# Kernel tuning notes

Measured on AMD Instinct MI355X. Metric: run time of the kernel, lower is better.

Reference implementation:

```python
import jax, jax.numpy as jnp
import numpy as np
import math

B, H, S, D = 2, 16, 2048, 64
DROP_P = 0.1


def setup_inputs() -> dict:
    key = jax.random.key(0)
    k1, k2 = jax.random.split(key)
    x1 = jax.random.normal(k1, (B, H, S, D), dtype=jnp.float32)  # queries
    x2 = jax.random.normal(k2, (B, H, S, D), dtype=jnp.float32)  # keys == values
    return {"x1": x1, "x2": x2}


def reference(x1, x2):
    # qk = x1 @ x2^T, scaled by 1/sqrt(head_dim)
    inv_scale = math.sqrt(x1.shape[-1])
    scores = jnp.einsum('bhqd,bhkd->bhqk', x1, x2) / inv_scale  # [B,H,S,S]
    probs = jax.nn.softmax(scores, axis=-1)
    # F.dropout(p=0.1) in training mode: deterministic jax mask with fixed key
    keep = jax.random.bernoulli(jax.random.key(42), 1.0 - DROP_P, probs.shape)
    probs = jnp.where(keep, probs / (1.0 - DROP_P), 0.0)
    out = jnp.einsum('bhqk,bhkd->bhqd', probs, x2)  # [B,H,S,D]
    return out
```

## Files before the change

### kernel.cpp

```cpp
#include <hip/hip_runtime.h>
#include <hip/hip_bf16.h>
#include <math.h>

#define BATCH 2
#define NHEAD 16
#define SLEN  2048
#define DH    64
#define WAVES 4
#define QW    16
#define QB    (WAVES*QW)
#define KB    64
#define PSTRIDE 68
#define MFIX  16.0f

typedef __attribute__((ext_vector_type(8))) short bf16x8;
typedef __attribute__((ext_vector_type(4))) float f32x4;

__device__ __forceinline__ unsigned rotl32(unsigned x, unsigned d) {
    return __builtin_amdgcn_alignbit(x, x, 32u - d);
}

__device__ __forceinline__ unsigned threefry_bits(unsigned i) {
    const unsigned k0 = 0u, k1 = 42u;
    const unsigned ks[3] = { k0, k1, k0 ^ k1 ^ 0x1BD11BDAu };
    unsigned x0 = 0u + ks[0];
    unsigned x1 = i  + ks[1];
#pragma unroll
    for (int g = 0; g < 5; ++g) {
        if ((g & 1) == 0) {
            x0 += x1; x1 = rotl32(x1, 13u); x1 ^= x0;
            x0 += x1; x1 = rotl32(x1, 15u); x1 ^= x0;
            x0 += x1; x1 = rotl32(x1, 26u); x1 ^= x0;
            x0 += x1; x1 = rotl32(x1,  6u); x1 ^= x0;
        } else {
            x0 += x1; x1 = rotl32(x1, 17u); x1 ^= x0;
            x0 += x1; x1 = rotl32(x1, 29u); x1 ^= x0;
            x0 += x1; x1 = rotl32(x1, 16u); x1 ^= x0;
            x0 += x1; x1 = rotl32(x1, 24u); x1 ^= x0;
        }
        x0 += ks[(g + 1) % 3];
        x1 += ks[(g + 2) % 3] + (unsigned)(g + 1);
    }
    return x0 ^ x1;
}

__device__ __forceinline__ int keep(unsigned flat) {
    return threefry_bits(flat) < 3865470464u;
}

__device__ __forceinline__ short f2bf(float f) {
    __hip_bfloat16 h = __float2bfloat16(f);
    return *reinterpret_cast<short*>(&h);
}

__global__ __launch_bounds__(256)
void attn_mfma_kernel(const float* __restrict__ Q,
                      const float* __restrict__ KV,
                      float* __restrict__ O) {
    __shared__ bf16x8 s_k[KB * 8];
    __shared__ bf16x8 s_vt[DH * 9];
    __shared__ float s_p[WAVES][QW][PSTRIDE];

    const int tid  = threadIdx.x;
    const int wave = tid >> 6;
    const int lane = tid & 63;
    const int g    = lane >> 4;
    const int lc   = lane & 15;

    const int blk = blockIdx.x;
    const int bh  = blk >> 5;
    const int q0  = (blk & 31) * QB + wave * QW;

    const float* Qb = Q  + ((size_t)bh * SLEN + q0) * DH;
    const float* Kb = KV + (size_t)bh * SLEN * DH;

    const float qscale = 0.125f * 1.4426950408889634f;
    bf16x8 qa[2];
#pragma unroll
    for (int h = 0; h < 2; ++h) {
        const float* qp = Qb + (size_t)lc * DH + 32 * h + g * 8;
        float4 f0 = *(const float4*)qp;
        float4 f1 = *(const float4*)(qp + 4);
        qa[h][0] = f2bf(f0.x * qscale); qa[h][1] = f2bf(f0.y * qscale);
        qa[h][2] = f2bf(f0.z * qscale); qa[h][3] = f2bf(f0.w * qscale);
        qa[h][4] = f2bf(f1.x * qscale); qa[h][5] = f2bf(f1.y * qscale);
        qa[h][6] = f2bf(f1.z * qscale); qa[h][7] = f2bf(f1.w * qscale);
    }

    f32x4 oacc[4];
#pragma unroll
    for (int t = 0; t < 4; ++t) oacc[t] = (f32x4){0.f, 0.f, 0.f, 0.f};
    float l[4] = { 0.f, 0.f, 0.f, 0.f };

    const unsigned rowbase = ((unsigned)bh * SLEN + (unsigned)(q0 + g * 4)) * SLEN;
    const unsigned fib = rowbase + (unsigned)lc;

    const int kr0 = tid >> 3;
    const int kc0 = tid & 7;
    const int vd  = tid & 63;
    const int vw  = tid >> 6;

    for (int k0 = 0; k0 < SLEN; k0 += KB) {
        __syncthreads();

#pragma unroll
        for (int rr = 0; rr < 2; ++rr) {
            const int row = kr0 + rr * 32;
            const float* src = Kb + (size_t)(k0 + row) * DH + kc0 * 8;
            float4 f0 = *(const float4*)src;
            float4 f1 = *(const float4*)(src + 4);
            bf16x8 v;
            v[0] = f2bf(f0.x); v[1] = f2bf(f0.y);
            v[2] = f2bf(f0.z); v[3] = f2bf(f0.w);
            v[4] = f2bf(f1.x); v[5] = f2bf(f1.y);
            v[6] = f2bf(f1.z); v[7] = f2bf(f1.w);
            s_k[row * 8 + (kc0 ^ (row & 7))] = v;
        }
#pragma unroll
        for (int rr = 0; rr < 2; ++rr) {
            const int w = vw + rr * 4;
            bf16x8 v;
#pragma unroll
            for (int j = 0; j < 8; ++j)
                v[j] = f2bf(Kb[(size_t)(k0 + w * 8 + j) * DH + vd]);
            s_vt[vd * 9 + w] = v;
        }
        __syncthreads();

        f32x4 sarr[4];
#pragma unroll
        for (int tt = 0; tt < 4; ++tt) {
            bf16x8 kb0 = s_k[(tt * 16 + lc) * 8 + (g       ^ (lc & 7))];
            bf16x8 kb1 = s_k[(tt * 16 + lc) * 8 + ((4 + g) ^ (lc & 7))];
            f32x4 acc = (f32x4){-MFIX, -MFIX, -MFIX, -MFIX};
            acc = __builtin_amdgcn_mfma_f32_16x16x32_bf16(qa[0], kb0, acc, 0, 0, 0);
            sarr[tt] = __builtin_amdgcn_mfma_f32_16x16x32_bf16(qa[1], kb1, acc, 0, 0, 0);
        }

#pragma unroll
        for (int i = 0; i < 4; ++i) {
            float p0 = __builtin_amdgcn_exp2f(sarr[0][i]);
            float p1 = __builtin_amdgcn_exp2f(sarr[1][i]);
            float p2 = __builtin_amdgcn_exp2f(sarr[2][i]);
            float p3 = __builtin_amdgcn_exp2f(sarr[3][i]);
            l[i] += (p0 + p1) + (p2 + p3);

            const unsigned fi = fib + (unsigned)i * SLEN + (unsigned)k0;
            if (!keep(fi))       p0 = 0.f;
            if (!keep(fi + 16u)) p1 = 0.f;
            if (!keep(fi + 32u)) p2 = 0.f;
            if (!keep(fi + 48u)) p3 = 0.f;
            float* pr = &s_p[wave][g * 4 + i][0];
            pr[lc]      = p0;
            pr[lc + 16] = p1;
            pr[lc + 32] = p2;
            pr[lc + 48] = p3;
        }

        const float* pp = &s_p[wave][lc][0];
        float4 pf0 = *(const float4*)(pp + g * 8);
        float4 pf1 = *(const float4*)(pp + g * 8 + 4);
        float4 pf2 = *(const float4*)(pp + 32 + g * 8);
        float4 pf3 = *(const float4*)(pp + 32 + g * 8 + 4);
        bf16x8 pa0, pa1;
        pa0[0] = f2bf(pf0.x); pa0[1] = f2bf(pf0.y);
        pa0[2] = f2bf(pf0.z); pa0[3] = f2bf(pf0.w);
        pa0[4] = f2bf(pf1.x); pa0[5] = f2bf(pf1.y);
        pa0[6] = f2bf(pf1.z); pa0[7] = f2bf(pf1.w);
        pa1[0] = f2bf(pf2.x); pa1[1] = f2bf(pf2.y);
        pa1[2] = f2bf(pf2.z); pa1[3] = f2bf(pf2.w);
        pa1[4] = f2bf(pf3.x); pa1[5] = f2bf(pf3.y);
        pa1[6] = f2bf(pf3.z); pa1[7] = f2bf(pf3.w);

#pragma unroll
        for (int t = 0; t < 4; ++t) {
            bf16x8 vb0 = s_vt[(t * 16 + lc) * 9 + g];
            bf16x8 vb1 = s_vt[(t * 16 + lc) * 9 + 4 + g];
            oacc[t] = __builtin_amdgcn_mfma_f32_16x16x32_bf16(pa0, vb0, oacc[t], 0, 0, 0);
            oacc[t] = __builtin_amdgcn_mfma_f32_16x16x32_bf16(pa1, vb1, oacc[t], 0, 0, 0);
        }
    }

#pragma unroll
    for (int i = 0; i < 4; ++i) {
        l[i] += __shfl_xor(l[i], 1);
        l[i] += __shfl_xor(l[i], 2);
        l[i] += __shfl_xor(l[i], 4);
        l[i] += __shfl_xor(l[i], 8);
    }

#pragma unroll
    for (int i = 0; i < 4; ++i) {
        float sc = 1.0f / (l[i] * 0.9f);
        float* orow = O + ((size_t)bh * SLEN + (size_t)(q0 + g * 4 + i)) * DH;
        orow[lc]      = oacc[0][i] * sc;
        orow[16 + lc] = oacc[1][i] * sc;
        orow[32 + lc] = oacc[2][i] * sc;
        orow[48 + lc] = oacc[3][i] * sc;
    }
}

extern "C" void kernel_launch(void* const* d_in, const int* in_sizes, int n_in,
                              void* d_out, int out_size, void* d_ws, size_t ws_size,
                              hipStream_t stream) {
    const float* x1 = (const float*)d_in[0];
    const float* x2 = (const float*)d_in[1];
    float* out = (float*)d_out;
    const int nblocks = BATCH * NHEAD * (SLEN / QB);
    attn_mfma_kernel<<<dim3(nblocks), dim3(256), 0, stream>>>(x1, x2, out);
}
```

Before: 298.0 us.

## Prefetch next K/V tile into registers and stage P as bf16 in LDS

Global loads of the next 64-key K/V tile are issued into registers right after the current tile is written to shared memory, so their latency overlaps the QK^T, softmax/dropout and PV work. The probability tile is converted to bf16 before the shared-memory store and read back as bf16x8 vectors, halving LDS traffic and removing per-element conversions after the readback. The prefetch adds register pressure, which may lower occupancy, and the last iteration does a wasted reload of tile 0.

```diff
diff --git a/kernel.cpp b/kernel.cpp
--- a/kernel.cpp
+++ b/kernel.cpp
@@ -10,7 +10,7 @@
 #define QW    16
 #define QB    (WAVES*QW)
 #define KB    64
-#define PSTRIDE 68
+#define PSTR  72
 #define MFIX  16.0f
 
 typedef __attribute__((ext_vector_type(8))) short bf16x8;
@@ -59,7 +59,7 @@
                       float* __restrict__ O) {
     __shared__ bf16x8 s_k[KB * 8];
     __shared__ bf16x8 s_vt[DH * 9];
-    __shared__ float s_p[WAVES][QW][PSTRIDE];
+    __shared__ __align__(16) short s_p[WAVES][QW][PSTR];
 
     const int tid  = threadIdx.x;
     const int wave = tid >> 6;
@@ -100,20 +100,38 @@
     const int vd  = tid & 63;
     const int vw  = tid >> 6;
 
+    float4 kpre[2][2];
+    float  vpre[2][8];
+
+    auto LOADT = [&](int kt) {
+#pragma unroll
+        for (int rr = 0; rr < 2; ++rr) {
+            const float* src = Kb + (size_t)(kt + kr0 + rr * 32) * DH + kc0 * 8;
+            kpre[rr][0] = *(const float4*)src;
+            kpre[rr][1] = *(const float4*)(src + 4);
+        }
+#pragma unroll
+        for (int rr = 0; rr < 2; ++rr) {
+            const int w = vw + rr * 4;
+#pragma unroll
+            for (int j = 0; j < 8; ++j)
+                vpre[rr][j] = Kb[(size_t)(kt + w * 8 + j) * DH + vd];
+        }
+    };
+
+    LOADT(0);
+
     for (int k0 = 0; k0 < SLEN; k0 += KB) {
         __syncthreads();
 
 #pragma unroll
         for (int rr = 0; rr < 2; ++rr) {
             const int row = kr0 + rr * 32;
-            const float* src = Kb + (size_t)(k0 + row) * DH + kc0 * 8;
-            float4 f0 = *(const float4*)src;
-            float4 f1 = *(const float4*)(src + 4);
             bf16x8 v;
-            v[0] = f2bf(f0.x); v[1] = f2bf(f0.y);
-            v[2] = f2bf(f0.z); v[3] = f2bf(f0.w);
-            v[4] = f2bf(f1.x); v[5] = f2bf(f1.y);
-            v[6] = f2bf(f1.z); v[7] = f2bf(f1.w);
+            v[0] = f2bf(kpre[rr][0].x); v[1] = f2bf(kpre[rr][0].y);
+            v[2] = f2bf(kpre[rr][0].z); v[3] = f2bf(kpre[rr][0].w);
+            v[4] = f2bf(kpre[rr][1].x); v[5] = f2bf(kpre[rr][1].y);
+            v[6] = f2bf(kpre[rr][1].z); v[7] = f2bf(kpre[rr][1].w);
             s_k[row * 8 + (kc0 ^ (row & 7))] = v;
         }
 #pragma unroll
@@ -121,10 +139,13 @@
             const int w = vw + rr * 4;
             bf16x8 v;
 #pragma unroll
-            for (int j = 0; j < 8; ++j)
-                v[j] = f2bf(Kb[(size_t)(k0 + w * 8 + j) * DH + vd]);
+            for (int j = 0; j < 8; ++j) v[j] = f2bf(vpre[rr][j]);
             s_vt[vd * 9 + w] = v;
         }
+
+        const int kn = (k0 + KB < SLEN) ? (k0 + KB) : 0;
+        LOADT(kn);
+
         __syncthreads();
 
         f32x4 sarr[4];
@@ -150,27 +171,15 @@
             if (!keep(fi + 16u)) p1 = 0.f;
             if (!keep(fi + 32u)) p2 = 0.f;
             if (!keep(fi + 48u)) p3 = 0.f;
-            float* pr = &s_p[wave][g * 4 + i][0];
-            pr[lc]      = p0;
-            pr[lc + 16] = p1;
-            pr[lc + 32] = p2;
-            pr[lc + 48] = p3;
-        }
-
-        const float* pp = &s_p[wave][lc][0];
-        float4 pf0 = *(const float4*)(pp + g * 8);
-        float4 pf1 = *(const float4*)(pp + g * 8 + 4);
-        float4 pf2 = *(const float4*)(pp + 32 + g * 8);
-        float4 pf3 = *(const float4*)(pp + 32 + g * 8 + 4);
-        bf16x8 pa0, pa1;
-        pa0[0] = f2bf(pf0.x); pa0[1] = f2bf(pf0.y);
-        pa0[2] = f2bf(pf0.z); pa0[3] = f2bf(pf0.w);
-        pa0[4] = f2bf(pf1.x); pa0[5] = f2bf(pf1.y);
-        pa0[6] = f2bf(pf1.z); pa0[7] = f2bf(pf1.w);
-        pa1[0] = f2bf(pf2.x); pa1[1] = f2bf(pf2.y);
-        pa1[2] = f2bf(pf2.z); pa1[3] = f2bf(pf2.w);
-        pa1[4] = f2bf(pf3.x); pa1[5] = f2bf(pf3.y);
-        pa1[6] = f2bf(pf3.z); pa1[7] = f2bf(pf3.w);
+            short* pr = &s_p[wave][g * 4 + i][0];
+            pr[lc]      = f2bf(p0);
+            pr[lc + 16] = f2bf(p1);
+            pr[lc + 32] = f2bf(p2);
+            pr[lc + 48] = f2bf(p3);
+        }
+
+        bf16x8 pa0 = *(const bf16x8*)&s_p[wave][lc][g * 8];
+        bf16x8 pa1 = *(const bf16x8*)&s_p[wave][lc][32 + g * 8];
 
 #pragma unroll
         for (int t = 0; t < 4; ++t) {
```

Result: faster. 278.2 us (-6.6%).
